# Kernel optimization log

Hardware: AMD Instinct MI355X
Metric: run time of the kernel (lower is better)

The kernel has to match this reference:

```python
import jax, jax.numpy as jnp
import numpy as np

N = 10000   # nodes
E = 160000  # edges (avg degree 16)
IN = 512
HID = 512
OUT = 512


def setup_inputs() -> dict:
    key = jax.random.key(0)
    ks = jax.random.split(key, 8)
    x = jax.random.normal(ks[0], (N, IN), dtype=jnp.float32)
    edge_index = jax.random.randint(ks[1], (2, E), 0, N, dtype=jnp.int64)
    def w(k, fi, fo):
        return jax.random.normal(k, (fi, fo), dtype=jnp.float32) * (1.0 / np.sqrt(fi)).astype(np.float32)
    return {
        "x": x,
        "edge_index": edge_index,
        "W1": w(ks[2], IN, HID), "b1": jnp.zeros((HID,), jnp.float32),
        "W2": w(ks[3], HID, HID), "b2": jnp.zeros((HID,), jnp.float32),
        "W3": w(ks[4], HID, OUT), "b3": jnp.zeros((OUT,), jnp.float32),
    }


def _gcn_norm(edge_index, n):
    # add self loops, then symmetric normalization D^{-1/2} (A+I) D^{-1/2}
    loops = jnp.arange(n, dtype=edge_index.dtype)
    row = jnp.concatenate([edge_index[0], loops])  # source
    col = jnp.concatenate([edge_index[1], loops])  # target (aggregation dim)
    deg = jax.ops.segment_sum(jnp.ones_like(col, jnp.float32), col, num_segments=n)
    dis = jnp.where(deg > 0, jax.lax.rsqrt(jnp.maximum(deg, 1.0)), 0.0)
    norm = dis[row] * dis[col]  # [E+N]
    return row, col, norm


def _gcn_layer(x, row, col, norm, W, b, n):
    h = x @ W                                    # [N, d_out] dense GEMM
    msg = h[row] * norm[:, None]                 # gather + scale, [E+N, d_out]
    out = jax.ops.segment_sum(msg, col, num_segments=n)  # scatter-add
    return out + b


def reference(x, edge_index, W1, b1, W2, b2, W3, b3):
    n = x.shape[0]
    row, col, norm = _gcn_norm(edge_index, n)
    h = _gcn_layer(x, row, col, norm, W1, b1, n)
    h = jax.nn.relu(h)  # dropout is identity in eval mode
    h = _gcn_layer(h, row, col, norm, W2, b2, n)
    h = jax.nn.relu(h)
    h = _gcn_layer(h, row, col, norm, W3, b3, n)
    return h
```

## Files before the change

kernel.cpp:

```cpp
#include <hip/hip_runtime.h>

typedef __attribute__((ext_vector_type(8))) short bf16x8;
typedef __attribute__((ext_vector_type(4))) float f32x4;

#define N_NODES 10000
#define N_EDGES 160000
#define FDIM    512
#define ELL     64
#define BM 64
#define BN 128
#define BK 64
#define TM 157
#define NGEMM (TM * 4)
#define NSCAT 625
#define NTRAN 768
#define NZERO 40
#define SLICES 4
#define SLW 128
#define SLB 2500

__device__ __forceinline__ float bf2f(unsigned int u) {
    union { unsigned int i; float f; } v; v.i = u << 16; return v.f;
}
__device__ __forceinline__ unsigned short f2bf(float f) {
    union { float f; unsigned int u; } v; v.f = f;
    unsigned int u = v.u;
    unsigned int r = u + 0x7fffu + ((u >> 16) & 1u);
    return (unsigned short)(r >> 16);
}
__device__ __forceinline__ void gload_lds16(const void* g, void* l) {
    __builtin_amdgcn_global_load_lds(
        (const __attribute__((address_space(1))) unsigned int*)g,
        (__attribute__((address_space(3))) unsigned int*)l, 16, 0, 0);
}
__device__ __forceinline__ int wave_is_f32(const unsigned int* w) {
    unsigned int v = w[(size_t)(threadIdx.x & 63) * 1000];
    unsigned int ex = (v >> 7) & 0xFFu;
    unsigned long long inb = __ballot(ex >= 100u && ex <= 140u);
    return (__popcll(inb) >= 48) ? 0 : 1;
}

__global__ __launch_bounds__(256) void prep_v9(
        const void* __restrict__ x, const void* __restrict__ ei,
        const void* __restrict__ W1, const void* __restrict__ W2,
        const void* __restrict__ W3, unsigned short* __restrict__ Wt,
        int* __restrict__ cnt, int* __restrict__ flags) {
    int b = blockIdx.x, tid = threadIdx.x;
    if (b < NTRAN) {
        __shared__ unsigned short tile[32][33];
        int z = b >> 8, t = b & 255;
        const void* W = (z == 0) ? W1 : (z == 1) ? W2 : W3;
        unsigned short* outp = Wt + (size_t)z * FDIM * FDIM;
        int ff32 = wave_is_f32((const unsigned int*)W);
        int tx = tid & 31, ty = tid >> 5;
        int xcol = (t & 15) * 32 + tx;
        int y0 = (t >> 4) * 32 + ty;
        #pragma unroll
        for (int j = 0; j < 32; j += 8) {
            int idx = (y0 + j) * FDIM + xcol;
            tile[ty + j][tx] = ff32 ? f2bf(((const float*)W)[idx])
                                    : ((const unsigned short*)W)[idx];
        }
        __syncthreads();
        int x2 = (t >> 4) * 32 + tx;
        int y2 = (t & 15) * 32 + ty;
        #pragma unroll
        for (int j = 0; j < 32; j += 8)
            outp[(y2 + j) * FDIM + x2] = tile[tx][ty + j];
    } else if (b < NTRAN + NZERO) {
        int i = (b - NTRAN) * 256 + tid;
        if (i < N_NODES) cnt[i] = 0;
    } else {
        if (tid < 64) {
            const unsigned long long* e64 = (const unsigned long long*)ei;
            unsigned long long v = e64[(size_t)tid * 2500];
            unsigned long long big = __ballot(v > 0xFFFFFFFFull);
            const unsigned int* xw = (const unsigned int*)x;
            unsigned int w = xw[(size_t)tid * 1000];
            unsigned int ex = (w >> 7) & 0xFFu;
            unsigned long long inb = __ballot(ex >= 100u && ex <= 140u);
            if (tid == 0) {
                flags[0] = (big == 0ull) ? 1 : 0;
                flags[1] = (__popcll(inb) >= 48) ? 0 : 1;
            }
        }
    }
}

__global__ __launch_bounds__(256) void gemm_v9(
        const void* __restrict__ Ap, const unsigned short* __restrict__ Bt,
        unsigned short* __restrict__ C, int a_ext,
        const int* __restrict__ flags, const void* __restrict__ ei,
        int* __restrict__ cnt, int* __restrict__ ell) {
    __shared__ unsigned short As[BM * BK];
    __shared__ unsigned short Bs[BN * BK];
    if (blockIdx.x >= NGEMM) {
        int e = (blockIdx.x - NGEMM) * 256 + threadIdx.x;
        if (e < N_EDGES) {
            int r, c;
            if (flags[0]) {
                r = (int)((const long long*)ei)[e];
                c = (int)((const long long*)ei)[N_EDGES + e];
            } else {
                r = ((const int*)ei)[e];
                c = ((const int*)ei)[N_EDGES + e];
            }
            int slot = atomicAdd(&cnt[c], 1);
            if (slot < ELL) ell[(size_t)c * ELL + slot] = r;
        }
        return;
    }
    const int K = FDIM;
    const int af32 = a_ext ? flags[1] : 0;
    const int tid = threadIdx.x;
    const int t = blockIdx.x;
    const int bm = (t % TM) * BM, bn = (t / TM) * BN;
    const int lane = tid & 63, wv = tid >> 6;
    const int wm = (wv >> 1) * 32, wn = (wv & 1) * 64;
    const int lrow = lane & 15;
    const int tsl = lane >> 4;
    const int ksw = (lane & 7) ^ ((lane >> 3) & 7);
    const unsigned short* Abf = (const unsigned short*)Ap;
    f32x4 acc[2][4] = {};

    for (int k0 = 0; k0 < K; k0 += BK) {
        if (!af32) {
            #pragma unroll
            for (int j = 0; j < 2; ++j) {
                int r0 = wv * 16 + j * 8;
                int arow = bm + r0 + (lane >> 3);
                if (arow >= N_NODES) arow = N_NODES - 1;
                gload_lds16(Abf + (size_t)arow * K + k0 + ksw * 8, &As[r0 * BK]);
            }
            #pragma unroll
            for (int j = 0; j < 4; ++j) {
                int r0 = wv * 32 + j * 8;
                gload_lds16(Bt + (size_t)(bn + r0 + (lane >> 3)) * K + k0 + ksw * 8,
                            &Bs[r0 * BK]);
            }
        } else {
            #pragma unroll
            for (int j = 0; j < 4; ++j) {
                int r0 = wv * 32 + j * 8;
                gload_lds16(Bt + (size_t)(bn + r0 + (lane >> 3)) * K + k0 + ksw * 8,
                            &Bs[r0 * BK]);
            }
            #pragma unroll
            for (int i = 0; i < 2; ++i) {
                int c = tid + i * 256;
                int row = c >> 3, sl = c & 7;
                int grow = bm + row;
                bf16x8 va = {};
                if (grow < N_NODES) {
                    const float* Af = (const float*)Ap + (size_t)grow * K + k0 + sl * 8;
                    f32x4 lo = *(const f32x4*)Af;
                    f32x4 hi = *(const f32x4*)(Af + 4);
                    #pragma unroll
                    for (int jj = 0; jj < 4; ++jj) {
                        va[jj]     = (short)f2bf(lo[jj]);
                        va[4 + jj] = (short)f2bf(hi[jj]);
                    }
                }
                *(bf16x8*)(&As[row * BK + ((sl ^ (row & 7)) * 8)]) = va;
            }
        }
        __syncthreads();
        #pragma unroll
        for (int half = 0; half < 2; ++half) {
            int ts = half * 4 + tsl;
            bf16x8 af[2], bfr[4];
            #pragma unroll
            for (int f = 0; f < 2; ++f) {
                int row = wm + f * 16 + lrow;
                af[f] = *(const bf16x8*)(&As[row * BK + ((ts ^ (lrow & 7)) * 8)]);
            }
            #pragma unroll
            for (int f = 0; f < 4; ++f) {
                int row = wn + f * 16 + lrow;
                bfr[f] = *(const bf16x8*)(&Bs[row * BK + ((ts ^ (lrow & 7)) * 8)]);
            }
            #pragma unroll
            for (int fm = 0; fm < 2; ++fm)
                #pragma unroll
                for (int fn = 0; fn < 4; ++fn)
                    acc[fm][fn] = __builtin_amdgcn_mfma_f32_16x16x32_bf16(
                        af[fm], bfr[fn], acc[fm][fn], 0, 0, 0);
        }
        __syncthreads();
    }

    int crow = (lane >> 4) * 4;
    int ccol = lane & 15;
    #pragma unroll
    for (int fm = 0; fm < 2; ++fm)
        #pragma unroll
        for (int fn = 0; fn < 4; ++fn)
            #pragma unroll
            for (int r = 0; r < 4; ++r) {
                int row = bm + wm + fm * 16 + crow + r;
                if (row < N_NODES)
                    C[(size_t)row * FDIM + bn + wn + fn * 16 + ccol] =
                        f2bf(acc[fm][fn][r]);
            }
}

__global__ __launch_bounds__(256) void agg_sl_v9(
        const unsigned short* __restrict__ gin, const void* __restrict__ bias,
        const int* __restrict__ cnt, const int* __restrict__ ell,
        void* __restrict__ out, int relu, int out_ext,
        const int* __restrict__ flags) {
    const int wv = threadIdx.x >> 6, lane = threadIdx.x & 63;
    const int slice = blockIdx.x / SLB;
    const int i = (blockIdx.x % SLB) * 4 + wv;
    const int fu = slice * (SLW / 2) + lane;
    const unsigned int* g32 = (const unsigned int*)gin;
    int ci = cnt[i];
    int re = (ci > ELL) ? ELL : ci;
    const int* ep = ell + (size_t)i * ELL;
    int   srcl = (lane < re) ? ep[lane] : 0;
    int   cl   = (lane < re) ? cnt[srcl] : 0;
    float wl   = rsqrtf((float)(cl + 1) * (float)(ci + 1));
    float a0 = 0.f, a1 = 0.f;
    int j = 0;
    for (; j + 8 <= re; j += 8) {
        int s0 = __shfl(srcl, j);     float w0 = __shfl(wl, j);
        int s1 = __shfl(srcl, j + 1); float w1 = __shfl(wl, j + 1);
        int s2 = __shfl(srcl, j + 2); float w2 = __shfl(wl, j + 2);
        int s3 = __shfl(srcl, j + 3); float w3 = __shfl(wl, j + 3);
        int s4 = __shfl(srcl, j + 4); float w4 = __shfl(wl, j + 4);
        int s5 = __shfl(srcl, j + 5); float w5 = __shfl(wl, j + 5);
        int s6 = __shfl(srcl, j + 6); float w6 = __shfl(wl, j + 6);
        int s7 = __shfl(srcl, j + 7); float w7 = __shfl(wl, j + 7);
        unsigned int v0 = g32[(size_t)s0 * 256 + fu];
        unsigned int v1 = g32[(size_t)s1 * 256 + fu];
        unsigned int v2 = g32[(size_t)s2 * 256 + fu];
        unsigned int v3 = g32[(size_t)s3 * 256 + fu];
        unsigned int v4 = g32[(size_t)s4 * 256 + fu];
        unsigned int v5 = g32[(size_t)s5 * 256 + fu];
        unsigned int v6 = g32[(size_t)s6 * 256 + fu];
        unsigned int v7 = g32[(size_t)s7 * 256 + fu];
        a0 += w0 * bf2f(v0 & 0xffffu); a1 += w0 * bf2f(v0 >> 16);
        a0 += w1 * bf2f(v1 & 0xffffu); a1 += w1 * bf2f(v1 >> 16);
        a0 += w2 * bf2f(v2 & 0xffffu); a1 += w2 * bf2f(v2 >> 16);
        a0 += w3 * bf2f(v3 & 0xffffu); a1 += w3 * bf2f(v3 >> 16);
        a0 += w4 * bf2f(v4 & 0xffffu); a1 += w4 * bf2f(v4 >> 16);
        a0 += w5 * bf2f(v5 & 0xffffu); a1 += w5 * bf2f(v5 >> 16);
        a0 += w6 * bf2f(v6 & 0xffffu); a1 += w6 * bf2f(v6 >> 16);
        a0 += w7 * bf2f(v7 & 0xffffu); a1 += w7 * bf2f(v7 >> 16);
    }
    for (; j < re; ++j) {
        int s = __shfl(srcl, j); float w = __shfl(wl, j);
        unsigned int v = g32[(size_t)s * 256 + fu];
        a0 += w * bf2f(v & 0xffffu); a1 += w * bf2f(v >> 16);
    }
    float wself = 1.0f / (float)(ci + 1);
    unsigned int vs = g32[(size_t)i * 256 + fu];
    a0 += wself * bf2f(vs & 0xffffu); a1 += wself * bf2f(vs >> 16);
    int ff32 = flags[1];
    if (ff32) {
        const float* B = (const float*)bias + fu * 2;
        a0 += B[0]; a1 += B[1];
    } else {
        unsigned int bb = ((const unsigned int*)bias)[fu];
        a0 += bf2f(bb & 0xffffu); a1 += bf2f(bb >> 16);
    }
    if (relu) { a0 = fmaxf(a0, 0.f); a1 = fmaxf(a1, 0.f); }
    if (out_ext && ff32) {
        float2 o = {a0, a1};
        *(float2*)((float*)out + (size_t)i * FDIM + fu * 2) = o;
    } else {
        unsigned int o = (unsigned int)f2bf(a0) | ((unsigned int)f2bf(a1) << 16);
        ((unsigned int*)out)[(size_t)i * 256 + fu] = o;
    }
}

extern "C" void kernel_launch(void* const* d_in, const int* in_sizes, int n_in,
                              void* d_out, int out_size, void* d_ws, size_t ws_size,
                              hipStream_t stream) {
    (void)in_sizes; (void)n_in; (void)out_size; (void)ws_size;
    const void* x  = d_in[0];
    const void* ei = d_in[1];
    const void* W1 = d_in[2];
    const void* b1 = d_in[3];
    const void* W2 = d_in[4];
    const void* b2 = d_in[5];
    const void* W3 = d_in[6];
    const void* b3 = d_in[7];

    char* p = (char*)d_ws;
    auto alloc = [&](size_t bytes) -> void* {
        void* r = (void*)p;
        p += (bytes + 255) & ~(size_t)255;
        return r;
    };
    int*  flags = (int*) alloc(16);
    int*  cnt   = (int*) alloc((size_t)N_NODES * 4);
    int*  ell   = (int*) alloc((size_t)N_NODES * ELL * 4);
    unsigned short* Wt = (unsigned short*)alloc((size_t)3 * FDIM * FDIM * 2);
    unsigned short* g  = (unsigned short*)alloc((size_t)N_NODES * FDIM * 2);

    unsigned short* Wt1 = Wt;
    unsigned short* Wt2 = Wt + (size_t)FDIM * FDIM;
    unsigned short* Wt3 = Wt + (size_t)2 * FDIM * FDIM;
    unsigned short* h   = (unsigned short*)d_out;

    prep_v9<<<NTRAN + NZERO + 1, 256, 0, stream>>>(x, ei, W1, W2, W3, Wt, cnt, flags);
    gemm_v9<<<NGEMM + NSCAT, 256, 0, stream>>>(x, Wt1, g, 1, flags, ei, cnt, ell);
    agg_sl_v9<<<SLICES * SLB, 256, 0, stream>>>(g, b1, cnt, ell, h, 1, 0, flags);
    gemm_v9<<<NGEMM, 256, 0, stream>>>(h, Wt2, g, 0, flags, ei, cnt, ell);
    agg_sl_v9<<<SLICES * SLB, 256, 0, stream>>>(g, b2, cnt, ell, h, 1, 0, flags);
    gemm_v9<<<NGEMM, 256, 0, stream>>>(h, Wt3, g, 0, flags, ei, cnt, ell);
    agg_sl_v9<<<SLICES * SLB, 256, 0, stream>>>(g, b3, cnt, ell, d_out, 0, 1, flags);
}
```

Before: 207.7 us.

## Overlap W2/W3 transpose with first GEMM and cache packed edge weights

Moves the W2/W3 transpose-and-convert blocks out of the prep kernel and into the first GEMM launch as extra blocks, so they run alongside the GEMM and edge scatter and the prep kernel gets shorter. The first aggregation now writes a packed (source, weight) ELL array. Layers 2 and 3 read that array directly instead of recomputing neighbour counts, rsqrt weights and shuffles. This adds an 8-byte-per-slot side array and extra global writes in layer 1, in exchange for less work per edge in later layers.

```diff
diff --git a/kernel.cpp b/kernel.cpp
--- a/kernel.cpp
+++ b/kernel.cpp
@@ -13,7 +13,8 @@
 #define TM 157
 #define NGEMM (TM * 4)
 #define NSCAT 625
-#define NTRAN 768
+#define NTR1  256
+#define NTR23 512
 #define NZERO 40
 #define SLICES 4
 #define SLW 128
@@ -40,35 +41,37 @@
     return (__popcll(inb) >= 48) ? 0 : 1;
 }
 
-__global__ __launch_bounds__(256) void prep_v9(
+__device__ __forceinline__ void tr_tile(const void* W, unsigned short* outp,
+                                        int t, int tid, void* ldsbuf) {
+    unsigned short (*tile)[33] = (unsigned short (*)[33])ldsbuf;
+    int ff32 = wave_is_f32((const unsigned int*)W);
+    int tx = tid & 31, ty = tid >> 5;
+    int xcol = (t & 15) * 32 + tx;
+    int y0 = (t >> 4) * 32 + ty;
+    #pragma unroll
+    for (int j = 0; j < 32; j += 8) {
+        int idx = (y0 + j) * FDIM + xcol;
+        tile[ty + j][tx] = ff32 ? f2bf(((const float*)W)[idx])
+                                : ((const unsigned short*)W)[idx];
+    }
+    __syncthreads();
+    int x2 = (t >> 4) * 32 + tx;
+    int y2 = (t & 15) * 32 + ty;
+    #pragma unroll
+    for (int j = 0; j < 32; j += 8)
+        outp[(y2 + j) * FDIM + x2] = tile[tx][ty + j];
+}
+
+__global__ __launch_bounds__(256) void prep_v10(
         const void* __restrict__ x, const void* __restrict__ ei,
-        const void* __restrict__ W1, const void* __restrict__ W2,
-        const void* __restrict__ W3, unsigned short* __restrict__ Wt,
+        const void* __restrict__ W1, unsigned short* __restrict__ Wt,
         int* __restrict__ cnt, int* __restrict__ flags) {
+    __shared__ unsigned short tile[32][33];
     int b = blockIdx.x, tid = threadIdx.x;
-    if (b < NTRAN) {
-        __shared__ unsigned short tile[32][33];
-        int z = b >> 8, t = b & 255;
-        const void* W = (z == 0) ? W1 : (z == 1) ? W2 : W3;
-        unsigned short* outp = Wt + (size_t)z * FDIM * FDIM;
-        int ff32 = wave_is_f32((const unsigned int*)W);
-        int tx = tid & 31, ty = tid >> 5;
-        int xcol = (t & 15) * 32 + tx;
-        int y0 = (t >> 4) * 32 + ty;
-        #pragma unroll
-        for (int j = 0; j < 32; j += 8) {
-            int idx = (y0 + j) * FDIM + xcol;
-            tile[ty + j][tx] = ff32 ? f2bf(((const float*)W)[idx])
-                                    : ((const unsigned short*)W)[idx];
-        }
-        __syncthreads();
-        int x2 = (t >> 4) * 32 + tx;
-        int y2 = (t & 15) * 32 + ty;
-        #pragma unroll
-        for (int j = 0; j < 32; j += 8)
-            outp[(y2 + j) * FDIM + x2] = tile[tx][ty + j];
-    } else if (b < NTRAN + NZERO) {
-        int i = (b - NTRAN) * 256 + tid;
+    if (b < NTR1) {
+        tr_tile(W1, Wt, b, tid, tile);
+    } else if (b < NTR1 + NZERO) {
+        int i = (b - NTR1) * 256 + tid;
         if (i < N_NODES) cnt[i] = 0;
     } else {
         if (tid < 64) {
@@ -87,26 +90,36 @@
     }
 }
 
-__global__ __launch_bounds__(256) void gemm_v9(
+__global__ __launch_bounds__(256) void gemm_v10(
         const void* __restrict__ Ap, const unsigned short* __restrict__ Bt,
         unsigned short* __restrict__ C, int a_ext,
         const int* __restrict__ flags, const void* __restrict__ ei,
-        int* __restrict__ cnt, int* __restrict__ ell) {
+        int* __restrict__ cnt, int* __restrict__ ell,
+        const void* __restrict__ W2, const void* __restrict__ W3,
+        unsigned short* __restrict__ Wt23) {
     __shared__ unsigned short As[BM * BK];
     __shared__ unsigned short Bs[BN * BK];
     if (blockIdx.x >= NGEMM) {
-        int e = (blockIdx.x - NGEMM) * 256 + threadIdx.x;
-        if (e < N_EDGES) {
-            int r, c;
-            if (flags[0]) {
-                r = (int)((const long long*)ei)[e];
-                c = (int)((const long long*)ei)[N_EDGES + e];
-            } else {
-                r = ((const int*)ei)[e];
-                c = ((const int*)ei)[N_EDGES + e];
-            }
-            int slot = atomicAdd(&cnt[c], 1);
-            if (slot < ELL) ell[(size_t)c * ELL + slot] = r;
+        int tb = blockIdx.x - NGEMM;
+        if (tb < NSCAT) {
+            int e = tb * 256 + threadIdx.x;
+            if (e < N_EDGES) {
+                int r, c;
+                if (flags[0]) {
+                    r = (int)((const long long*)ei)[e];
+                    c = (int)((const long long*)ei)[N_EDGES + e];
+                } else {
+                    r = ((const int*)ei)[e];
+                    c = ((const int*)ei)[N_EDGES + e];
+                }
+                int slot = atomicAdd(&cnt[c], 1);
+                if (slot < ELL) ell[(size_t)c * ELL + slot] = r;
+            }
+        } else {
+            int t = tb - NSCAT;
+            int z = t >> 8;
+            tr_tile(z ? W3 : W2, Wt23 + (size_t)z * FDIM * FDIM, t & 255,
+                    threadIdx.x, As);
         }
         return;
     }
@@ -204,10 +217,10 @@
             }
 }
 
-__global__ __launch_bounds__(256) void agg_sl_v9(
+__global__ __launch_bounds__(256) void agg_build_v10(
         const unsigned short* __restrict__ gin, const void* __restrict__ bias,
         const int* __restrict__ cnt, const int* __restrict__ ell,
-        void* __restrict__ out, int relu, int out_ext,
+        int2* __restrict__ ell2, void* __restrict__ out,
         const int* __restrict__ flags) {
     const int wv = threadIdx.x >> 6, lane = threadIdx.x & 63;
     const int slice = blockIdx.x / SLB;
@@ -220,6 +233,10 @@
     int   srcl = (lane < re) ? ep[lane] : 0;
     int   cl   = (lane < re) ? cnt[srcl] : 0;
     float wl   = rsqrtf((float)(cl + 1) * (float)(ci + 1));
+    if (slice == 0 && lane < re) {
+        int2 pk; pk.x = srcl; pk.y = __float_as_int(wl);
+        ell2[(size_t)i * ELL + lane] = pk;
+    }
     float a0 = 0.f, a1 = 0.f;
     int j = 0;
     for (; j + 8 <= re; j += 8) {
@@ -256,6 +273,66 @@
     float wself = 1.0f / (float)(ci + 1);
     unsigned int vs = g32[(size_t)i * 256 + fu];
     a0 += wself * bf2f(vs & 0xffffu); a1 += wself * bf2f(vs >> 16);
+    if (flags[1]) {
+        const float* B = (const float*)bias + fu * 2;
+        a0 += B[0]; a1 += B[1];
+    } else {
+        unsigned int bb = ((const unsigned int*)bias)[fu];
+        a0 += bf2f(bb & 0xffffu); a1 += bf2f(bb >> 16);
+    }
+    a0 = fmaxf(a0, 0.f); a1 = fmaxf(a1, 0.f);
+    unsigned int o = (unsigned int)f2bf(a0) | ((unsigned int)f2bf(a1) << 16);
+    ((unsigned int*)out)[(size_t)i * 256 + fu] = o;
+}
+
+__global__ __launch_bounds__(256) void agg_use_v10(
+        const unsigned short* __restrict__ gin, const void* __restrict__ bias,
+        const int* __restrict__ cnt, const int2* __restrict__ ell2,
+        void* __restrict__ out, int relu, int out_ext,
+        const int* __restrict__ flags) {
+    const int wv = threadIdx.x >> 6, lane = threadIdx.x & 63;
+    const int slice = blockIdx.x / SLB;
+    const int i = (blockIdx.x % SLB) * 4 + wv;
+    const int fu = slice * (SLW / 2) + lane;
+    const unsigned int* g32 = (const unsigned int*)gin;
+    int ci = cnt[i];
+    int re = (ci > ELL) ? ELL : ci;
+    const int2* ep = ell2 + (size_t)i * ELL;
+    float a0 = 0.f, a1 = 0.f;
+    int j = 0;
+    for (; j + 8 <= re; j += 8) {
+        int2 p0 = ep[j],     p1 = ep[j + 1], p2 = ep[j + 2], p3 = ep[j + 3];
+        int2 p4 = ep[j + 4], p5 = ep[j + 5], p6 = ep[j + 6], p7 = ep[j + 7];
+        unsigned int v0 = g32[(size_t)p0.x * 256 + fu];
+        unsigned int v1 = g32[(size_t)p1.x * 256 + fu];
+        unsigned int v2 = g32[(size_t)p2.x * 256 + fu];
+        unsigned int v3 = g32[(size_t)p3.x * 256 + fu];
+        unsigned int v4 = g32[(size_t)p4.x * 256 + fu];
+        unsigned int v5 = g32[(size_t)p5.x * 256 + fu];
+        unsigned int v6 = g32[(size_t)p6.x * 256 + fu];
+        unsigned int v7 = g32[(size_t)p7.x * 256 + fu];
+        float w0 = __int_as_float(p0.y), w1 = __int_as_float(p1.y);
+        float w2 = __int_as_float(p2.y), w3 = __int_as_float(p3.y);
+        float w4 = __int_as_float(p4.y), w5 = __int_as_float(p5.y);
+        float w6 = __int_as_float(p6.y), w7 = __int_as_float(p7.y);
+        a0 += w0 * bf2f(v0 & 0xffffu); a1 += w0 * bf2f(v0 >> 16);
+        a0 += w1 * bf2f(v1 & 0xffffu); a1 += w1 * bf2f(v1 >> 16);
+        a0 += w2 * bf2f(v2 & 0xffffu); a1 += w2 * bf2f(v2 >> 16);
+        a0 += w3 * bf2f(v3 & 0xffffu); a1 += w3 * bf2f(v3 >> 16);
+        a0 += w4 * bf2f(v4 & 0xffffu); a1 += w4 * bf2f(v4 >> 16);
+        a0 += w5 * bf2f(v5 & 0xffffu); a1 += w5 * bf2f(v5 >> 16);
+        a0 += w6 * bf2f(v6 & 0xffffu); a1 += w6 * bf2f(v6 >> 16);
+        a0 += w7 * bf2f(v7 & 0xffffu); a1 += w7 * bf2f(v7 >> 16);
+    }
+    for (; j < re; ++j) {
+        int2 pp = ep[j];
+        float w = __int_as_float(pp.y);
+        unsigned int v = g32[(size_t)pp.x * 256 + fu];
+        a0 += w * bf2f(v & 0xffffu); a1 += w * bf2f(v >> 16);
+    }
+    float wself = 1.0f / (float)(ci + 1);
+    unsigned int vs = g32[(size_t)i * 256 + fu];
+    a0 += wself * bf2f(vs & 0xffffu); a1 += wself * bf2f(vs >> 16);
     int ff32 = flags[1];
     if (ff32) {
         const float* B = (const float*)bias + fu * 2;
@@ -296,6 +373,7 @@
     int*  flags = (int*) alloc(16);
     int*  cnt   = (int*) alloc((size_t)N_NODES * 4);
     int*  ell   = (int*) alloc((size_t)N_NODES * ELL * 4);
+    int2* ell2  = (int2*)alloc((size_t)N_NODES * ELL * 8);
     unsigned short* Wt = (unsigned short*)alloc((size_t)3 * FDIM * FDIM * 2);
     unsigned short* g  = (unsigned short*)alloc((size_t)N_NODES * FDIM * 2);
 
@@ -304,11 +382,14 @@
     unsigned short* Wt3 = Wt + (size_t)2 * FDIM * FDIM;
     unsigned short* h   = (unsigned short*)d_out;
 
-    prep_v9<<<NTRAN + NZERO + 1, 256, 0, stream>>>(x, ei, W1, W2, W3, Wt, cnt, flags);
-    gemm_v9<<<NGEMM + NSCAT, 256, 0, stream>>>(x, Wt1, g, 1, flags, ei, cnt, ell);
-    agg_sl_v9<<<SLICES * SLB, 256, 0, stream>>>(g, b1, cnt, ell, h, 1, 0, flags);
-    gemm_v9<<<NGEMM, 256, 0, stream>>>(h, Wt2, g, 0, flags, ei, cnt, ell);
-    agg_sl_v9<<<SLICES * SLB, 256, 0, stream>>>(g, b2, cnt, ell, h, 1, 0, flags);
-    gemm_v9<<<NGEMM, 256, 0, stream>>>(h, Wt3, g, 0, flags, ei, cnt, ell);
-    agg_sl_v9<<<SLICES * SLB, 256, 0, stream>>>(g, b3, cnt, ell, d_out, 0, 1, flags);
-}
+    prep_v10<<<NTR1 + NZERO + 1, 256, 0, stream>>>(x, ei, W1, Wt1, cnt, flags);
+    gemm_v10<<<NGEMM + NSCAT + NTR23, 256, 0, stream>>>(
+        x, Wt1, g, 1, flags, ei, cnt, ell, W2, W3, Wt2);
+    agg_build_v10<<<SLICES * SLB, 256, 0, stream>>>(g, b1, cnt, ell, ell2, h, flags);
+    gemm_v10<<<NGEMM, 256, 0, stream>>>(h, Wt2, g, 0, flags, ei, cnt, ell,
+                                        W2, W3, Wt2);
+    agg_use_v10<<<SLICES * SLB, 256, 0, stream>>>(g, b2, cnt, ell2, h, 1, 0, flags);
+    gemm_v10<<<NGEMM, 256, 0, stream>>>(h, Wt3, g, 0, flags, ei, cnt, ell,
+                                        W2, W3, Wt2);
+    agg_use_v10<<<SLICES * SLB, 256, 0, stream>>>(g, b3, cnt, ell2, d_out, 0, 1, flags);
+}
```

New measurement: 219.2 us. 5.5% more time.
